# Kernel tuning notes

Hardware: AMD Instinct MI355X
Metric: run time of the kernel (lower is better)

## Reference

```python
import jax, jax.numpy as jnp
import numpy as np

B, CI, HW, K, C, NH, L = 512, 3, 28, 28 // 28 and 0 or 7, 1024, 16, 12
K = 7


def setup_inputs() -> dict:
    key = jax.random.key(0)
    ks = jax.random.split(key, 8)
    s = 0.02
    return {
        "x": jax.random.normal(ks[0], (B, CI, HW, HW), jnp.float32),
        "conv_w": jax.random.normal(ks[1], (C, CI, K, K), jnp.float32) * s,  # Conv2d weight [Co,Ci,k,k], shared with deconv
        "ln1_w": jnp.ones((L, C), jnp.float32),
        "ln1_b": jnp.zeros((L, C), jnp.float32),
        "wq": jax.random.normal(ks[2], (L, C, C), jnp.float32) * s,
        "wk": jax.random.normal(ks[3], (L, C, C), jnp.float32) * s,
        "wv": jax.random.normal(ks[4], (L, C, C), jnp.float32) * s,
        "ln2_w": jnp.ones((L, C), jnp.float32),
        "ln2_b": jnp.zeros((L, C), jnp.float32),
        "mlp_w": jax.random.normal(ks[5], (L, C, C), jnp.float32) * s,
        "mlp_b": jnp.zeros((L, C), jnp.float32),
        "out_w": jax.random.normal(ks[6], (C, C), jnp.float32) * s,
        "out_b": jnp.zeros((C,), jnp.float32),
        "head_num": NH,
    }


def _layernorm(x, w, b, eps=1e-5):
    m = jnp.mean(x, axis=-1, keepdims=True)
    v = jnp.var(x, axis=-1, keepdims=True)  # biased var, matches torch LayerNorm
    return (x - m) * jax.lax.rsqrt(v + eps) * w + b


def _attn(h, wq, wk, wv, nh):
    b, t, c = h.shape
    hd = c // nh
    q = (h @ wq.T).reshape(b, t, nh, hd).transpose(0, 2, 1, 3)  # [B,H,T,hd]
    k = (h @ wk.T).reshape(b, t, nh, hd).transpose(0, 2, 1, 3)
    v = (h @ wv.T).reshape(b, t, nh, hd).transpose(0, 2, 1, 3)
    scores = jnp.einsum("bhqd,bhkd->bhqk", q, k) / jnp.sqrt(jnp.float32(hd))
    mask = jnp.tril(jnp.ones((t, t), bool))
    scores = jnp.where(mask, scores, -jnp.inf)
    a = jax.nn.softmax(scores, axis=-1)
    o = jnp.einsum("bhqk,bhkd->bhqd", a, v)
    return o.transpose(0, 2, 1, 3).reshape(b, t, c)


def _forward(x, conv_w, ln1_w, ln1_b, wq, wk, wv, ln2_w, ln2_b, mlp_w, mlp_b, out_w, out_b, head_num):
    b, ci, hh, ww = x.shape
    co, _, k, _ = conv_w.shape
    # thumbnail: bilinear downsample to (k,k) (align_corners=False == half-pixel), then k-strided conv -> [B,Co]
    thumb = jax.image.resize(x, (b, ci, k, k), method="bilinear", antialias=False)
    thumb_tok = jnp.einsum("bcpq,dcpq->bd", thumb, conv_w)
    # kernel==stride conv == patchify + matmul
    hp, wp = hh // k, ww // k
    xp = x.reshape(b, ci, hp, k, wp, k)
    patches = jnp.einsum("bcipjq,dcpq->bdij", xp, conv_w).reshape(b, co, hp * wp)
    h = jnp.concatenate([thumb_tok[:, :, None], patches], axis=-1).transpose(0, 2, 1)  # [B,T=1+hp*wp,C]
    nlayers = ln1_w.shape[0]
    for l in range(nlayers):
        a = _attn(_layernorm(h, ln1_w[l], ln1_b[l]), wq[l], wk[l], wv[l], head_num)
        h = h + a
        m = _layernorm(h, ln2_w[l], ln2_b[l]) @ mlp_w[l].T + mlp_b[l]
        h = h + m
    logits = h @ out_w.T + out_b  # [B,T,C]
    # decode: ConvTranspose2d(kernel=stride=k) with shared weight; input [B,Co,1,T] -> [B,Ci,k,T*k]
    z = logits.transpose(0, 2, 1)  # [B,Co,T]
    t = z.shape[-1]
    out = jnp.einsum("bcs,cdhw->bdhsw", z, conv_w).reshape(b, ci, k, t * k)
    return out


def reference(x, conv_w, ln1_w, ln1_b, wq, wk, wv, ln2_w, ln2_b, mlp_w, mlp_b, out_w, out_b, head_num):
    return _forward(x, conv_w, ln1_w, ln1_b, wq, wk, wv, ln2_w, ln2_b, mlp_w, mlp_b, out_w, out_b, head_num)
```

## Files before the change

kernel.cpp:

```cpp
#include <hip/hip_runtime.h>


typedef unsigned short u16;
typedef short bfrag8 __attribute__((ext_vector_type(8)));
typedef float facc4 __attribute__((ext_vector_type(4)));

__device__ __forceinline__ u16 f2bf(float f) {
  union { float f; unsigned u; } x; x.f = f;
  unsigned r = x.u + 0x7fffu + ((x.u >> 16) & 1u);
  return (u16)(r >> 16);
}
__device__ __forceinline__ float bf2f(u16 h) {
  union { unsigned u; float f; } x; x.u = ((unsigned)h) << 16;
  return x.f;
}

template <int MODE>
__global__ __launch_bounds__(256) void gemm_bt(
    const u16* __restrict__ A, int lda,
    const u16* __restrict__ B0, const u16* __restrict__ B1, const u16* __restrict__ B2,
    int ldb, int K, int NX,
    void* __restrict__ outp, long long zstride, int ldo,
    const float* __restrict__ bias)
{
  __shared__ __align__(16) u16 As[8192];
  __shared__ __align__(16) u16 Bs[8192];

  const int l = blockIdx.x;
  const int xcd = l & 7;
  const int j = l >> 3;
  const int per_epoch = 9 * NX;
  const int z = j / per_epoch;
  const int r2 = j - z * per_epoch;
  const int g = r2 / NX;
  const int y = xcd + 8 * g;
  if (y >= 68) return;
  const int x = r2 - g * NX;
  const int n0 = x * 128;
  const int m0 = y * 128;
  const u16* __restrict__ B = (z == 0) ? B0 : ((z == 1) ? B1 : B2);

  const int tid  = threadIdx.x;
  const int wave = tid >> 6;
  const int lane = tid & 63;
  const int wm   = (wave >> 1) * 64;
  const int wn   = (wave & 1) * 64;
  const int lrow = lane & 15;
  const int lquad = lane >> 4;

  facc4 acc[4][4] = {};

  const u16* ga[4]; const u16* gb[4];
#pragma unroll
  for (int j2 = 0; j2 < 4; ++j2) {
    const int s = tid + 256 * j2;
    const int t = s >> 9, s2 = s & 511;
    const int r = s2 >> 2, c = (s2 & 3) + 4 * t;
    ga[j2] = A + (long long)(m0 + r) * lda + c * 8;
    gb[j2] = B + (long long)(n0 + r) * ldb + c * 8;
  }

  const int aoff = (wm + lrow) * 32 + lquad * 8;
  const int boff = (wn + lrow) * 32 + lquad * 8;

  for (int k0 = 0; k0 < K; k0 += 64) {
#pragma unroll
    for (int j2 = 0; j2 < 4; ++j2) {
      __builtin_amdgcn_global_load_lds((const __attribute__((address_space(1))) void*)ga[j2],
                                       (__attribute__((address_space(3))) void*)(As + (tid + 256 * j2) * 8), 16, 0, 0);
      __builtin_amdgcn_global_load_lds((const __attribute__((address_space(1))) void*)gb[j2],
                                       (__attribute__((address_space(3))) void*)(Bs + (tid + 256 * j2) * 8), 16, 0, 0);
      ga[j2] += 64; gb[j2] += 64;
    }
    __syncthreads();

#pragma unroll
    for (int t = 0; t < 2; ++t) {
      bfrag8 af[4], bfr[4];
#pragma unroll
      for (int im = 0; im < 4; ++im) af[im] = *(const bfrag8*)(As + t * 4096 + aoff + 512 * im);
#pragma unroll
      for (int in = 0; in < 4; ++in) bfr[in] = *(const bfrag8*)(Bs + t * 4096 + boff + 512 * in);
#pragma unroll
      for (int im = 0; im < 4; ++im)
#pragma unroll
        for (int in = 0; in < 4; ++in)
          acc[im][in] = __builtin_amdgcn_mfma_f32_16x16x32_bf16(af[im], bfr[in], acc[im][in], 0, 0, 0);
    }
    __syncthreads();
  }

#pragma unroll
  for (int in = 0; in < 4; ++in) {
    const int col = n0 + wn + in * 16 + lrow;
    const float bb = bias ? bias[col] : 0.0f;
#pragma unroll
    for (int im = 0; im < 4; ++im) {
#pragma unroll
      for (int r = 0; r < 4; ++r) {
        const int row = m0 + wm + im * 16 + lquad * 4 + r;
        const float v = acc[im][in][r] + bb;
        if (MODE == 0) {
          ((float*)outp)[(long long)row * ldo + col] = v;
        } else if (MODE == 1) {
          (((u16*)outp) + zstride * z)[(long long)row * ldo + col] = f2bf(v);
        } else if (MODE == 2) {
          ((float*)outp)[(long long)row * ldo + col] += v;
        } else if (MODE == 4) {
          const long long off = (long long)row * ldo + col;
          const float nv = ((float*)outp)[off] + v;
          ((float*)outp)[off] = nv;
          ((u16*)zstride)[off] = f2bf(nv);
        } else {
          if (col < 147) {
            const int b = row / 17, s = row - b * 17;
            const int d = col / 49, rem = col - d * 49;
            const int hk = rem / 7, wk = rem - hk * 7;
            ((float*)outp)[(long long)((b * 3 + d) * 7 + hk) * 119 + s * 7 + wk] = v;
          }
        }
      }
    }
  }
}

__global__ __launch_bounds__(256) void ln_kernel(
    const float* __restrict__ h, const float* __restrict__ w,
    const float* __restrict__ b, u16* __restrict__ out)
{
  const long long row = blockIdx.x;
  const int t = threadIdx.x;
  const float4 v = ((const float4*)(h + row * 1024))[t];
  float s = v.x + v.y + v.z + v.w;
  float q = v.x * v.x + v.y * v.y + v.z * v.z + v.w * v.w;
  for (int o = 32; o > 0; o >>= 1) { s += __shfl_down(s, o); q += __shfl_down(q, o); }
  __shared__ float ss[4], sq[4];
  const int wave = t >> 6, lane = t & 63;
  if (lane == 0) { ss[wave] = s; sq[wave] = q; }
  __syncthreads();
  const float st = ss[0] + ss[1] + ss[2] + ss[3];
  const float qt = sq[0] + sq[1] + sq[2] + sq[3];
  const float mean = st * (1.0f / 1024.0f);
  const float var = qt * (1.0f / 1024.0f) - mean * mean;
  const float inv = rsqrtf(var + 1e-5f);
  const float4 w4 = ((const float4*)w)[t];
  const float4 b4 = ((const float4*)b)[t];
  ushort4 o;
  o.x = f2bf((v.x - mean) * inv * w4.x + b4.x);
  o.y = f2bf((v.y - mean) * inv * w4.y + b4.y);
  o.z = f2bf((v.z - mean) * inv * w4.z + b4.z);
  o.w = f2bf((v.w - mean) * inv * w4.w + b4.w);
  ((ushort4*)(out + row * 1024))[t] = o;
}

__global__ __launch_bounds__(256) void attn_kernel(const u16* __restrict__ QKV,
                                                   float* __restrict__ h)
{
  const int blk = blockIdx.x;
  const int b = blk >> 4, head = blk & 15;
  __shared__ float qs[17][64], ks[17][64], vs[17][64];
  __shared__ float sc[17][20];
  const long long base = (long long)b * 17408 + head * 64;
  const u16* Q  = QKV;
  const u16* Kp = QKV + 8912896LL;
  const u16* V  = QKV + 17825792LL;
  const int tid = threadIdx.x;

  if (tid < 136) {
    const int t = tid >> 3, dg = (tid & 7) * 8;
    const long long off = base + (long long)t * 1024 + dg;
    union { uint4 u; u16 s[8]; } xq, xk, xv;
    xq.u = *(const uint4*)(Q + off);
    xk.u = *(const uint4*)(Kp + off);
    xv.u = *(const uint4*)(V + off);
#pragma unroll
    for (int j = 0; j < 8; ++j) {
      qs[t][dg + j] = bf2f(xq.s[j]);
      ks[t][dg + j] = bf2f(xk.s[j]);
      vs[t][dg + j] = bf2f(xv.s[j]);
    }
  }
  __syncthreads();

  for (int i = tid; i < 289; i += 256) {
    const int tq = i / 17, tk = i % 17;
    float a = 0.0f;
    if (tk <= tq) {
#pragma unroll
      for (int d = 0; d < 64; ++d) a += qs[tq][d] * ks[tk][d];
      a *= 0.125f;
    }
    sc[tq][tk] = a;
  }
  __syncthreads();

  if (tid < 17) {
    const int tq = tid;
    float m = -1e30f;
    for (int tk = 0; tk <= tq; ++tk) m = fmaxf(m, sc[tq][tk]);
    float s = 0.0f;
    for (int tk = 0; tk <= tq; ++tk) { const float e = __expf(sc[tq][tk] - m); sc[tq][tk] = e; s += e; }
    const float inv = 1.0f / s;
    for (int tk = 0; tk <= tq; ++tk) sc[tq][tk] *= inv;
  }
  __syncthreads();

  for (int i = tid; i < 272; i += 256) {
    const int tq = i >> 4, dg = (i & 15) * 4;
    float o0 = 0, o1 = 0, o2 = 0, o3 = 0;
    for (int tk = 0; tk <= tq; ++tk) {
      const float s = sc[tq][tk];
      o0 += s * vs[tk][dg];     o1 += s * vs[tk][dg + 1];
      o2 += s * vs[tk][dg + 2]; o3 += s * vs[tk][dg + 3];
    }
    float4* hp = (float4*)(h + base + (long long)tq * 1024 + dg);
    float4 hv = *hp;
    hv.x += o0; hv.y += o1; hv.z += o2; hv.w += o3;
    *hp = hv;
  }
}

__global__ void build_p(const float* __restrict__ x, u16* __restrict__ P)
{
  const int n = blockIdx.x;
  const int j = threadIdx.x;
  if (j >= 192) return;
  const int b = n / 17, t = n % 17;
  float val = 0.0f;
  if (j < 147) {
    const int c = j / 49, rem = j % 49, p = rem / 7, q = rem % 7;
    const float* xb = x + (long long)(b * 3 + c) * 784;
    if (t == 0) {
      const int r = 4 * p + 1, cc = 4 * q + 1;
      val = 0.25f * (xb[r * 28 + cc] + xb[r * 28 + cc + 1] +
                     xb[(r + 1) * 28 + cc] + xb[(r + 1) * 28 + cc + 1]);
    } else {
      const int s = t - 1, ii = s >> 2, jj = s & 3;
      val = xb[(7 * ii + p) * 28 + 7 * jj + q];
    }
  }
  P[(long long)n * 192 + j] = f2bf(val);
}

__global__ __launch_bounds__(256) void cvt_conv(const float* __restrict__ cw,
                                                u16* __restrict__ Wc, u16* __restrict__ cw2)
{
  const int i = blockIdx.x * 256 + threadIdx.x;
  if (i < 196608) {
    const int d = i / 192, j = i % 192;
    Wc[i] = (j < 147) ? f2bf(cw[d * 147 + j]) : (u16)0;
  } else {
    const int i2 = i - 196608;
    if (i2 < 262144) {
      const int j = i2 / 1024, c = i2 % 1024;
      cw2[i2] = (j < 147) ? f2bf(cw[c * 147 + j]) : (u16)0;
    }
  }
}

__global__ __launch_bounds__(256) void wprime_kernel(
    const u16* __restrict__ cw2, const float* __restrict__ outw,
    u16* __restrict__ Wp)
{
  const int k = blockIdx.x * 256 + threadIdx.x;
  const int j = blockIdx.y;
  float a = 0.0f;
  for (int c = 0; c < 1024; ++c)
    a += bf2f(cw2[j * 1024 + c]) * outw[c * 1024 + k];
  Wp[j * 1024 + k] = f2bf(a);
}

__global__ __launch_bounds__(256) void bprime_kernel(
    const u16* __restrict__ cw2, const float* __restrict__ outb,
    float* __restrict__ bp)
{
  const int j = threadIdx.x;
  float a = 0.0f;
  for (int c = 0; c < 1024; ++c) a += outb[c] * bf2f(cw2[j * 1024 + c]);
  bp[j] = a;
}

__global__ __launch_bounds__(256) void cvt_all(
    const float* __restrict__ wq, const float* __restrict__ wk,
    const float* __restrict__ wv, const float* __restrict__ mlpw,
    const float* __restrict__ outw, u16* __restrict__ wAll)
{
  const int i = blockIdx.x * 256 + threadIdx.x;
  const int which = i >> 18;
  const int off = i & 262143;
  const float4* src;
  if (which < 48) {
    const int layer = which >> 2, sub = which & 3;
    const float* base = (sub == 0) ? wq : (sub == 1) ? wk : (sub == 2) ? wv : mlpw;
    src = (const float4*)(base + (size_t)layer * 1048576) + off;
  } else {
    src = (const float4*)outw + off;
  }
  const float4 v = *src;
  ushort4 o; o.x = f2bf(v.x); o.y = f2bf(v.y); o.z = f2bf(v.z); o.w = f2bf(v.w);
  *(ushort4*)(wAll + (size_t)which * 1048576 + (size_t)off * 4) = o;
}

__global__ __launch_bounds__(256) void cvt4(const float* __restrict__ a0, const float* __restrict__ a1,
                                            const float* __restrict__ a2, const float* __restrict__ a3,
                                            u16* __restrict__ o3, u16* __restrict__ om)
{
  const int i = blockIdx.x * 256 + threadIdx.x;
  const int which = i >> 20, off = i & 1048575;
  const float* src = (which == 0) ? a0 : (which == 1) ? a1 : (which == 2) ? a2 : a3;
  const float v = src[off];
  if (which < 3) o3[which * 1048576 + off] = f2bf(v);
  else           om[off] = f2bf(v);
}

__global__ __launch_bounds__(256) void cvtN(const float* __restrict__ in, u16* __restrict__ out, int n)
{
  const int i = blockIdx.x * 256 + threadIdx.x;
  if (i < n) out[i] = f2bf(in[i]);
}

extern "C" void kernel_launch(void* const* d_in, const int* in_sizes, int n_in,
                              void* d_out, int out_size, void* d_ws, size_t ws_size,
                              hipStream_t stream)
{
  const float* x     = (const float*)d_in[0];
  const float* convw = (const float*)d_in[1];
  const float* ln1w  = (const float*)d_in[2];
  const float* ln1b  = (const float*)d_in[3];
  const float* wq    = (const float*)d_in[4];
  const float* wk    = (const float*)d_in[5];
  const float* wv    = (const float*)d_in[6];
  const float* ln2w  = (const float*)d_in[7];
  const float* ln2b  = (const float*)d_in[8];
  const float* mlpw  = (const float*)d_in[9];
  const float* mlpb  = (const float*)d_in[10];
  const float* outw  = (const float*)d_in[11];
  const float* outb  = (const float*)d_in[12];

  char* w = (char*)d_ws;
  const bool big = (ws_size >= 214500352ULL);

  const int G_QKV = 8 * 3 * 9 * 8;
  const int G_ONE = 8 * 1 * 9 * 8;
  const int G_DEC = 8 * 1 * 9 * 2;

  if (big) {
    float* h   = (float*)(w);
    u16* Abuf  = (u16*)(w + 35651584);
    u16* QKV   = (u16*)(w + 53477376);
    u16* wAll  = (u16*)(w + 106954752);
    u16* Wc    = (u16*)(w + 209715200);
    u16* cw2   = (u16*)(w + 210108416);
    u16* P     = (u16*)(w + 210632704);
    u16* Wp    = (u16*)(w + 213975040);
    float* bp  = (float*)(w + 214499328);

    cvt_all<<<50176, 256, 0, stream>>>(wq, wk, wv, mlpw, outw, wAll);
    cvt_conv<<<1792, 256, 0, stream>>>(convw, Wc, cw2);
    wprime_kernel<<<dim3(4, 256), 256, 0, stream>>>(cw2, outw, Wp);
    bprime_kernel<<<1, 256, 0, stream>>>(cw2, outb, bp);
    build_p<<<8704, 192, 0, stream>>>(x, P);
    gemm_bt<0><<<G_ONE, 256, 0, stream>>>(P, 192, Wc, Wc, Wc, 192, 192, 8,
                                          (void*)h, 0LL, 1024, nullptr);
    for (int l = 0; l < 12; ++l) {
      u16* wl = wAll + (size_t)l * 4194304;
      ln_kernel<<<8704, 256, 0, stream>>>(h, ln1w + l * 1024, ln1b + l * 1024, Abuf);
      gemm_bt<1><<<G_QKV, 256, 0, stream>>>(Abuf, 1024, wl, wl + 1048576, wl + 2097152,
                                            1024, 1024, 8, (void*)QKV, 8912896LL, 1024, nullptr);
      attn_kernel<<<8192, 256, 0, stream>>>(QKV, h);
      ln_kernel<<<8704, 256, 0, stream>>>(h, ln2w + l * 1024, ln2b + l * 1024, Abuf);
      if (l < 11) {
        gemm_bt<2><<<G_ONE, 256, 0, stream>>>(Abuf, 1024, wl + 3145728, wl, wl,
                                              1024, 1024, 8, (void*)h, 0LL, 1024, mlpb + l * 1024);
      } else {
        gemm_bt<4><<<G_ONE, 256, 0, stream>>>(Abuf, 1024, wl + 3145728, wl, wl,
                                              1024, 1024, 8, (void*)h,
                                              (long long)(uintptr_t)QKV, 1024,
                                              mlpb + l * 1024);
      }
    }
    gemm_bt<3><<<G_DEC, 256, 0, stream>>>(QKV, 1024, Wp, Wp, Wp,
                                          1024, 1024, 2, d_out, 0LL, 0, bp);
  } else {
    if (ws_size < 119603200ULL) return;
    float* h   = (float*)(w);
    u16* Abuf  = (u16*)(w + 35651584);
    u16* QKV   = (u16*)(w + 53477376);
    u16* wb3   = (u16*)(w + 106954752);
    u16* wmb   = (u16*)(w + 113246208);
    u16* Wc    = (u16*)(w + 115343360);
    u16* cw2   = (u16*)(w + 115736576);
    u16* P     = (u16*)(w + 116260864);

    cvt_conv<<<1792, 256, 0, stream>>>(convw, Wc, cw2);
    build_p<<<8704, 192, 0, stream>>>(x, P);
    gemm_bt<0><<<G_ONE, 256, 0, stream>>>(P, 192, Wc, Wc, Wc, 192, 192, 8,
                                          (void*)h, 0LL, 1024, nullptr);
    for (int l = 0; l < 12; ++l) {
      const size_t wo = (size_t)l * 1048576;
      cvt4<<<16384, 256, 0, stream>>>(wq + wo, wk + wo, wv + wo, mlpw + wo, wb3, wmb);
      ln_kernel<<<8704, 256, 0, stream>>>(h, ln1w + l * 1024, ln1b + l * 1024, Abuf);
      gemm_bt<1><<<G_QKV, 256, 0, stream>>>(Abuf, 1024, wb3, wb3 + 1048576, wb3 + 2097152,
                                            1024, 1024, 8, (void*)QKV, 8912896LL, 1024, nullptr);
      attn_kernel<<<8192, 256, 0, stream>>>(QKV, h);
      ln_kernel<<<8704, 256, 0, stream>>>(h, ln2w + l * 1024, ln2b + l * 1024, Abuf);
      gemm_bt<2><<<G_ONE, 256, 0, stream>>>(Abuf, 1024, wmb, wmb, wmb,
                                            1024, 1024, 8, (void*)h, 0LL, 1024, mlpb + l * 1024);
    }
    cvtN<<<34816, 256, 0, stream>>>(h, Abuf, 8912896);
    cvtN<<<4096, 256, 0, stream>>>(outw, wmb, 1048576);
    gemm_bt<1><<<G_ONE, 256, 0, stream>>>(Abuf, 1024, wmb, wmb, wmb,
                                          1024, 1024, 8, (void*)QKV, 0LL, 1024, outb);
    gemm_bt<3><<<G_DEC, 256, 0, stream>>>(QKV, 1024, cw2, cw2, cw2,
                                          1024, 1024, 2, d_out, 0LL, 0, nullptr);
  }
}
```

Measured before the change: 2.777 ms.

## Add 256x256-tile 8-wave bf16 GEMM with LDS double-buffering for QKV and MLP

Adds a new gemm256 kernel that uses 256x256 output tiles with 512 threads. It stages A and B quarter-tiles into a double-buffered 128KB LDS region with global_load_lds, splits each K-step into four phases that interleave LDS fragment loads, next-tile prefetch and MFMA bursts at raised priority, and uses XCD-aware block remapping. The QKV projection and the MLP GEMMs (including the final fused bf16-copy epilogue) switch to it. The aim is more data reuse per tile and better overlap of loads with MFMA. The costs are larger tiles, which give fewer blocks (136 for the MLP GEMM, possibly under-filling CUs), uncoalesced epilogue stores, and high register pressure.

```diff
diff --git a/kernel.cpp b/kernel.cpp
--- a/kernel.cpp
+++ b/kernel.cpp
@@ -13,6 +13,199 @@
 __device__ __forceinline__ float bf2f(u16 h) {
   union { unsigned u; float f; } x; x.u = ((unsigned)h) << 16;
   return x.f;
+}
+
+
+template <int QM, int QN>
+__device__ __forceinline__ void phase_ldsload(const u16* S, int sb, int mh, int w4,
+                                              int aLane, bfrag8 (&af)[4][2], bfrag8 (&bf)[2][2])
+{
+  const int ab = sb + QM * 8192 + mh * 4096 + aLane;
+  const int bb = sb + 16384 + QN * 8192 + w4 * 2048 + aLane;
+#pragma unroll
+  for (int im = 0; im < 4; ++im)
+#pragma unroll
+    for (int kk = 0; kk < 2; ++kk)
+      af[im][kk] = *(const bfrag8*)&S[ab + im * 1024 + kk * 32];
+#pragma unroll
+  for (int in = 0; in < 2; ++in)
+#pragma unroll
+    for (int kk = 0; kk < 2; ++kk)
+      bf[in][kk] = *(const bfrag8*)&S[bb + in * 1024 + kk * 32];
+}
+
+template <int QM, int QN>
+__device__ __forceinline__ void phase_mfma(bfrag8 (&af)[4][2], bfrag8 (&bf)[2][2],
+                                           facc4 (&acc)[8][4])
+{
+#pragma unroll
+  for (int im = 0; im < 4; ++im)
+#pragma unroll
+    for (int in = 0; in < 2; ++in) {
+      facc4 c = acc[QM * 4 + im][QN * 2 + in];
+      c = __builtin_amdgcn_mfma_f32_16x16x32_bf16(af[im][0], bf[in][0], c, 0, 0, 0);
+      c = __builtin_amdgcn_mfma_f32_16x16x32_bf16(af[im][1], bf[in][1], c, 0, 0, 0);
+      acc[QM * 4 + im][QN * 2 + in] = c;
+    }
+}
+
+template <int MODE>
+__global__ __launch_bounds__(512, 2) void gemm256(
+    const u16* __restrict__ A, int lda,
+    const u16* __restrict__ B0, const u16* __restrict__ B1, const u16* __restrict__ B2,
+    int ldb, int K, int cpx,
+    void* __restrict__ outp, long long zstride, int ldo,
+    const float* __restrict__ bias)
+{
+  __shared__ u16 S[65536];
+
+  const int bid = blockIdx.x;
+  const int wg = (bid & 7) * cpx + (bid >> 3);
+  const int perz = 34 * 4;
+  const int z = wg / perz;
+  const int r0 = wg - z * perz;
+  const int y = r0 >> 2;
+  const int x = r0 & 3;
+  const int m0 = y * 256, n0 = x * 256;
+  const u16* __restrict__ B = (z == 0) ? B0 : ((z == 1) ? B1 : B2);
+
+  const int tid = threadIdx.x;
+  const int wave = tid >> 6;
+  const int lane = tid & 63;
+  const int lrow = lane & 15, lquad = lane >> 4;
+  const int mh = wave >> 2;
+  const int w4 = wave & 3;
+  const int wm = mh * 128, wn = w4 * 64;
+
+  const int swzE = ((lrow & 4) << 2) | (lrow & 8);
+  const int aLane = lrow * 64 + ((lquad * 8) ^ swzE);
+
+  const int l3 = lane >> 3;
+  const int ec = (lane & 7) * 8;
+  const int sw0 = (lane & 32) >> 1;
+  const int kc0 = ec ^ sw0;
+  const int kc1 = ec ^ sw0 ^ 8;
+  const int ch0 = wave * 2, ch1 = ch0 + 1;
+  const int arow0 = (ch0 >> 3) * 128 + ((ch0 & 7) * 8 + l3);
+  const int arow1 = (ch1 >> 3) * 128 + ((ch1 & 7) * 8 + l3);
+  const int brow0 = (ch0 >> 2) * 64 + ((ch0 & 3) * 8 + l3);
+  const int brow1 = (ch1 >> 2) * 64 + ((ch1 & 3) * 8 + l3);
+  const u16* gA0 = A + (long long)(m0 + arow0) * lda + kc0;
+  const u16* gA1 = A + (long long)(m0 + arow1) * lda + kc1;
+  const u16* gB0 = B + (long long)(n0 + brow0) * ldb + kc0;
+  const u16* gB1 = B + (long long)(n0 + brow1) * ldb + kc1;
+  const long long aq = 64LL * lda;
+  const long long bq = 32LL * ldb;
+  const int ldsW = wave * 1024 + lane * 8;
+
+  auto stageA = [&](int qm, int tt) {
+    u16* d0 = S + ((tt & 1) * 32768 + qm * 8192) + ldsW;
+    __builtin_amdgcn_global_load_lds((const __attribute__((address_space(1))) void*)(gA0 + qm * aq + tt * 64),
+                                     (__attribute__((address_space(3))) void*)d0, 16, 0, 0);
+    __builtin_amdgcn_global_load_lds((const __attribute__((address_space(1))) void*)(gA1 + qm * aq + tt * 64),
+                                     (__attribute__((address_space(3))) void*)(d0 + 512), 16, 0, 0);
+  };
+  auto stageB = [&](int qn, int tt) {
+    u16* d0 = S + ((tt & 1) * 32768 + 16384 + qn * 8192) + ldsW;
+    __builtin_amdgcn_global_load_lds((const __attribute__((address_space(1))) void*)(gB0 + qn * bq + tt * 64),
+                                     (__attribute__((address_space(3))) void*)d0, 16, 0, 0);
+    __builtin_amdgcn_global_load_lds((const __attribute__((address_space(1))) void*)(gB1 + qn * bq + tt * 64),
+                                     (__attribute__((address_space(3))) void*)(d0 + 512), 16, 0, 0);
+  };
+
+  facc4 acc[8][4] = {};
+
+  stageA(0, 0); stageB(0, 0); stageA(1, 0); stageB(1, 0); stageB(0, 1); stageA(0, 1);
+  asm volatile("s_waitcnt vmcnt(4)" ::: "memory");
+  __builtin_amdgcn_sched_barrier(0);
+  __builtin_amdgcn_s_barrier();
+
+  const int NT = K >> 6;
+  for (int t = 0; t < NT; ++t) {
+    const int sb = (t & 1) * 32768;
+    {
+      bfrag8 af[4][2], bf[2][2];
+      phase_ldsload<0, 0>(S, sb, mh, w4, aLane, af, bf);
+      if (t + 1 < NT) stageA(1, t + 1);
+      __builtin_amdgcn_sched_barrier(0);
+      __builtin_amdgcn_s_barrier();
+      asm volatile("s_waitcnt lgkmcnt(0)" ::: "memory");
+      __builtin_amdgcn_sched_barrier(0);
+      __builtin_amdgcn_s_setprio(1);
+      phase_mfma<0, 0>(af, bf, acc);
+      __builtin_amdgcn_s_setprio(0);
+      __builtin_amdgcn_sched_barrier(0);
+      __builtin_amdgcn_s_barrier();
+    }
+    {
+      bfrag8 af[4][2], bf[2][2];
+      phase_ldsload<1, 0>(S, sb, mh, w4, aLane, af, bf);
+      if (t + 1 < NT) stageB(1, t + 1);
+      __builtin_amdgcn_sched_barrier(0);
+      __builtin_amdgcn_s_barrier();
+      asm volatile("s_waitcnt lgkmcnt(0)" ::: "memory");
+      __builtin_amdgcn_sched_barrier(0);
+      __builtin_amdgcn_s_setprio(1);
+      phase_mfma<1, 0>(af, bf, acc);
+      __builtin_amdgcn_s_setprio(0);
+      __builtin_amdgcn_sched_barrier(0);
+      __builtin_amdgcn_s_barrier();
+    }
+    {
+      bfrag8 af[4][2], bf[2][2];
+      phase_ldsload<0, 1>(S, sb, mh, w4, aLane, af, bf);
+      if (t + 2 < NT) stageB(0, t + 2);
+      __builtin_amdgcn_sched_barrier(0);
+      __builtin_amdgcn_s_barrier();
+      asm volatile("s_waitcnt lgkmcnt(0)" ::: "memory");
+      __builtin_amdgcn_sched_barrier(0);
+      __builtin_amdgcn_s_setprio(1);
+      phase_mfma<0, 1>(af, bf, acc);
+      __builtin_amdgcn_s_setprio(0);
+      __builtin_amdgcn_sched_barrier(0);
+      __builtin_amdgcn_s_barrier();
+    }
+    {
+      bfrag8 af[4][2], bf[2][2];
+      phase_ldsload<1, 1>(S, sb, mh, w4, aLane, af, bf);
+      if (t + 2 < NT) stageA(0, t + 2);
+      __builtin_amdgcn_sched_barrier(0);
+      __builtin_amdgcn_s_barrier();
+      asm volatile("s_waitcnt lgkmcnt(0)" ::: "memory");
+      __builtin_amdgcn_sched_barrier(0);
+      __builtin_amdgcn_s_setprio(1);
+      phase_mfma<1, 1>(af, bf, acc);
+      __builtin_amdgcn_s_setprio(0);
+      if (t + 2 < NT) asm volatile("s_waitcnt vmcnt(4)" ::: "memory");
+      else            asm volatile("s_waitcnt vmcnt(0)" ::: "memory");
+      __builtin_amdgcn_sched_barrier(0);
+      __builtin_amdgcn_s_barrier();
+    }
+  }
+
+#pragma unroll
+  for (int in = 0; in < 4; ++in) {
+    const int col = n0 + wn + in * 16 + lrow;
+    const float bb = bias ? bias[col] : 0.0f;
+#pragma unroll
+    for (int im = 0; im < 8; ++im) {
+#pragma unroll
+      for (int r = 0; r < 4; ++r) {
+        const int row = m0 + wm + im * 16 + lquad * 4 + r;
+        const float v = acc[im][in][r] + bb;
+        if (MODE == 1) {
+          (((u16*)outp) + zstride * z)[(long long)row * ldo + col] = f2bf(v);
+        } else if (MODE == 2) {
+          ((float*)outp)[(long long)row * ldo + col] += v;
+        } else {
+          const long long off = (long long)row * ldo + col;
+          const float nv = ((float*)outp)[off] + v;
+          ((float*)outp)[off] = nv;
+          ((u16*)zstride)[off] = f2bf(nv);
+        }
+      }
+    }
+  }
 }
 
 template <int MODE>
@@ -365,18 +558,18 @@
     for (int l = 0; l < 12; ++l) {
       u16* wl = wAll + (size_t)l * 4194304;
       ln_kernel<<<8704, 256, 0, stream>>>(h, ln1w + l * 1024, ln1b + l * 1024, Abuf);
-      gemm_bt<1><<<G_QKV, 256, 0, stream>>>(Abuf, 1024, wl, wl + 1048576, wl + 2097152,
-                                            1024, 1024, 8, (void*)QKV, 8912896LL, 1024, nullptr);
+      gemm256<1><<<408, 512, 0, stream>>>(Abuf, 1024, wl, wl + 1048576, wl + 2097152,
+                                          1024, 1024, 51, (void*)QKV, 8912896LL, 1024, nullptr);
       attn_kernel<<<8192, 256, 0, stream>>>(QKV, h);
       ln_kernel<<<8704, 256, 0, stream>>>(h, ln2w + l * 1024, ln2b + l * 1024, Abuf);
       if (l < 11) {
-        gemm_bt<2><<<G_ONE, 256, 0, stream>>>(Abuf, 1024, wl + 3145728, wl, wl,
-                                              1024, 1024, 8, (void*)h, 0LL, 1024, mlpb + l * 1024);
+        gemm256<2><<<136, 512, 0, stream>>>(Abuf, 1024, wl + 3145728, wl + 3145728, wl + 3145728,
+                                            1024, 1024, 17, (void*)h, 0LL, 1024, mlpb + l * 1024);
       } else {
-        gemm_bt<4><<<G_ONE, 256, 0, stream>>>(Abuf, 1024, wl + 3145728, wl, wl,
-                                              1024, 1024, 8, (void*)h,
-                                              (long long)(uintptr_t)QKV, 1024,
-                                              mlpb + l * 1024);
+        gemm256<4><<<136, 512, 0, stream>>>(Abuf, 1024, wl + 3145728, wl + 3145728, wl + 3145728,
+                                            1024, 1024, 17, (void*)h,
+                                            (long long)(uintptr_t)QKV, 1024,
+                                            mlpb + l * 1024);
       }
     }
     gemm_bt<3><<<G_DEC, 256, 0, stream>>>(QKV, 1024, Wp, Wp, Wp,
```

After: 3.891 ms. 1.4x slower.

## Use 256x256-tile triple-buffered GEMM kernel for QKV projection

Applied to the files above, without the earlier changes.

Adds a new 512-thread GEMM kernel with 256x256 output tiles, three-stage LDS buffering fed by direct global-to-LDS loads, swizzled LDS layout, and XCD-aware block remapping. The QKV projection in each layer now uses it instead of the older gemm_bt kernel. The larger tile is meant to raise arithmetic intensity and cut global traffic per MFMA, while the deeper pipeline hides load latency. In exchange it uses 96KB of LDS and more registers per block, which lowers occupancy. The grid has exactly 408 blocks, which may leave some compute units unevenly loaded.

```diff
diff --git a/kernel.cpp b/kernel.cpp
--- a/kernel.cpp
+++ b/kernel.cpp
@@ -13,6 +13,171 @@
 __device__ __forceinline__ float bf2f(u16 h) {
   union { unsigned u; float f; } x; x.u = ((unsigned)h) << 16;
   return x.f;
+}
+
+
+template <int MODE>
+__global__ __launch_bounds__(512, 2) void gemm256(
+    const u16* __restrict__ A, int lda,
+    const u16* __restrict__ B0, const u16* __restrict__ B1, const u16* __restrict__ B2,
+    int ldb, int K, int cpx,
+    void* __restrict__ outp, long long zstride, int ldo,
+    const float* __restrict__ bias)
+{
+  __shared__ u16 S[49152];
+
+  const int bid = blockIdx.x;
+  const int wg = (bid & 7) * cpx + (bid >> 3);
+  const int perz = 34 * 4;
+  const int z = wg / perz;
+  const int r0 = wg - z * perz;
+  const int y = r0 >> 2;
+  const int x = r0 & 3;
+  const int m0 = y * 256, n0 = x * 256;
+  const u16* __restrict__ B = (z == 0) ? B0 : ((z == 1) ? B1 : B2);
+
+  const int tid = threadIdx.x;
+  const int wave = tid >> 6;
+  const int lane = tid & 63;
+  const int lrow = lane & 15, lquad = lane >> 4;
+  const int mh = wave >> 2;
+  const int w4 = wave & 3;
+  const int wm = mh * 128, wn = w4 * 64;
+
+  int offA[4], offB[2];
+#pragma unroll
+  for (int im = 0; im < 4; ++im) {
+    const int rr = mh * 64 + im * 16 + lrow;
+    const int l = rr >> 1;
+    const int s = (lquad + 4 * (rr & 1)) ^ (l & 7);
+    offA[im] = l * 64 + s * 8;
+  }
+#pragma unroll
+  for (int in = 0; in < 2; ++in) {
+    const int rr = w4 * 32 + in * 16 + lrow;
+    const int l = rr >> 1;
+    const int s = (lquad + 4 * (rr & 1)) ^ (l & 7);
+    offB[in] = l * 64 + s * 8;
+  }
+
+  const int rgn = wave >> 1;
+  const int hh = wave & 1;
+  const u16* gsrc[4];
+  int gdst[4];
+#pragma unroll
+  for (int i = 0; i < 4; ++i) {
+    const int p = hh * 256 + i * 64 + lane;
+    const int l = p >> 3, s = p & 7;
+    const int v = s ^ (l & 7);
+    const int rrs = 2 * l + (v >> 2);
+    const int cs = v & 3;
+    if (rgn < 2) {
+      const int grow = m0 + (rrs >> 6) * 128 + rgn * 64 + (rrs & 63);
+      gsrc[i] = A + (long long)grow * lda + cs * 8;
+    } else {
+      const int gcol = n0 + (rrs >> 5) * 64 + (rgn - 2) * 32 + (rrs & 31);
+      gsrc[i] = B + (long long)gcol * ldb + cs * 8;
+    }
+    gdst[i] = rgn * 4096 + p * 8;
+  }
+
+  facc4 acc[8][4] = {};
+
+#pragma unroll
+  for (int i = 0; i < 4; ++i) {
+    __builtin_amdgcn_global_load_lds((const __attribute__((address_space(1))) void*)gsrc[i],
+                                     (__attribute__((address_space(3))) void*)(S + gdst[i]), 16, 0, 0);
+    gsrc[i] += 32;
+  }
+#pragma unroll
+  for (int i = 0; i < 4; ++i) {
+    __builtin_amdgcn_global_load_lds((const __attribute__((address_space(1))) void*)gsrc[i],
+                                     (__attribute__((address_space(3))) void*)(S + 16384 + gdst[i]), 16, 0, 0);
+    gsrc[i] += 32;
+  }
+  asm volatile("s_waitcnt vmcnt(4)" ::: "memory");
+  __builtin_amdgcn_sched_barrier(0);
+  __builtin_amdgcn_s_barrier();
+  __builtin_amdgcn_sched_barrier(0);
+
+  const int NT = K >> 5;
+  int sb0 = 0, sb1 = 16384, sb2 = 32768;
+
+  for (int t = 0; t < NT; ++t) {
+    bfrag8 a0[4], a1[4], bf0[2], bf1[2];
+#pragma unroll
+    for (int im = 0; im < 4; ++im) a0[im] = *(const bfrag8*)&S[sb0 + offA[im]];
+#pragma unroll
+    for (int in = 0; in < 2; ++in) bf0[in] = *(const bfrag8*)&S[sb0 + 8192 + offB[in]];
+#pragma unroll
+    for (int in = 0; in < 2; ++in) bf1[in] = *(const bfrag8*)&S[sb0 + 12288 + offB[in]];
+#pragma unroll
+    for (int im = 0; im < 4; ++im) a1[im] = *(const bfrag8*)&S[sb0 + 4096 + offA[im]];
+    if (t + 2 < NT) {
+#pragma unroll
+      for (int i = 0; i < 4; ++i) {
+        __builtin_amdgcn_global_load_lds((const __attribute__((address_space(1))) void*)gsrc[i],
+                                         (__attribute__((address_space(3))) void*)(S + sb2 + gdst[i]), 16, 0, 0);
+        gsrc[i] += 32;
+      }
+    }
+    __builtin_amdgcn_s_setprio(1);
+#pragma unroll
+    for (int im = 0; im < 4; ++im)
+#pragma unroll
+      for (int in = 0; in < 2; ++in)
+        acc[im][in] = __builtin_amdgcn_mfma_f32_16x16x32_bf16(a0[im], bf0[in], acc[im][in], 0, 0, 0);
+#pragma unroll
+    for (int im = 0; im < 4; ++im)
+#pragma unroll
+      for (int in = 0; in < 2; ++in)
+        acc[im][2 + in] = __builtin_amdgcn_mfma_f32_16x16x32_bf16(a0[im], bf1[in], acc[im][2 + in], 0, 0, 0);
+#pragma unroll
+    for (int im = 0; im < 4; ++im)
+#pragma unroll
+      for (int in = 0; in < 2; ++in)
+        acc[4 + im][2 + in] = __builtin_amdgcn_mfma_f32_16x16x32_bf16(a1[im], bf1[in], acc[4 + im][2 + in], 0, 0, 0);
+#pragma unroll
+    for (int im = 0; im < 4; ++im)
+#pragma unroll
+      for (int in = 0; in < 2; ++in)
+        acc[4 + im][in] = __builtin_amdgcn_mfma_f32_16x16x32_bf16(a1[im], bf0[in], acc[4 + im][in], 0, 0, 0);
+    __builtin_amdgcn_s_setprio(0);
+
+    if (t + 1 < NT) {
+      __builtin_amdgcn_sched_barrier(0);
+      if (t + 2 < NT) asm volatile("s_waitcnt vmcnt(4)" ::: "memory");
+      else            asm volatile("s_waitcnt vmcnt(0)" ::: "memory");
+      __builtin_amdgcn_sched_barrier(0);
+      __builtin_amdgcn_s_barrier();
+      __builtin_amdgcn_sched_barrier(0);
+    }
+    const int tmp = sb0; sb0 = sb1; sb1 = sb2; sb2 = tmp;
+  }
+
+#pragma unroll
+  for (int in = 0; in < 4; ++in) {
+    const int col = n0 + wn + in * 16 + lrow;
+    const float bb = bias ? bias[col] : 0.0f;
+#pragma unroll
+    for (int im = 0; im < 8; ++im) {
+#pragma unroll
+      for (int r = 0; r < 4; ++r) {
+        const int row = m0 + wm + im * 16 + lquad * 4 + r;
+        const float v = acc[im][in][r] + bb;
+        if (MODE == 1) {
+          (((u16*)outp) + zstride * z)[(long long)row * ldo + col] = f2bf(v);
+        } else if (MODE == 2) {
+          ((float*)outp)[(long long)row * ldo + col] += v;
+        } else {
+          const long long off = (long long)row * ldo + col;
+          const float nv = ((float*)outp)[off] + v;
+          ((float*)outp)[off] = nv;
+          ((u16*)zstride)[off] = f2bf(nv);
+        }
+      }
+    }
+  }
 }
 
 template <int MODE>
@@ -365,8 +530,8 @@
     for (int l = 0; l < 12; ++l) {
       u16* wl = wAll + (size_t)l * 4194304;
       ln_kernel<<<8704, 256, 0, stream>>>(h, ln1w + l * 1024, ln1b + l * 1024, Abuf);
-      gemm_bt<1><<<G_QKV, 256, 0, stream>>>(Abuf, 1024, wl, wl + 1048576, wl + 2097152,
-                                            1024, 1024, 8, (void*)QKV, 8912896LL, 1024, nullptr);
+      gemm256<1><<<408, 512, 0, stream>>>(Abuf, 1024, wl, wl + 1048576, wl + 2097152,
+                                          1024, 1024, 51, (void*)QKV, 8912896LL, 1024, nullptr);
       attn_kernel<<<8192, 256, 0, stream>>>(QKV, h);
       ln_kernel<<<8704, 256, 0, stream>>>(h, ln2w + l * 1024, ln2b + l * 1024, Abuf);
       if (l < 11) {
```

Result: faster. 2.681 ms (-3.4%).
